# Kernel optimization log

Hardware: AMD Instinct MI355X
Metric: run time of the kernel (lower is better)

Reference implementation:

```python
import jax, jax.numpy as jnp
import numpy as np

N = 262144          # total views (rows of x)
G = 65536           # number of objects / view-groups (len(n_views))
D_IN, D_MID, D_GAT, D_OUT = 512, 256, 128, 256
BN_EPS = 1e-5
L2_EPS = 1e-9


def setup_inputs() -> dict:
    key = jax.random.key(0)
    ks = jax.random.split(key, 12)
    # post-backbone pooled features (dla34 last stage -> AdaptiveMaxPool2d(1) -> flatten)
    x = jax.random.normal(ks[0], (N, D_IN), jnp.float32)
    # ragged grouping: sorted segment ids, every segment guaranteed non-empty
    extra = jax.random.randint(ks[1], (N - G,), 0, G)
    seg_ids = jnp.sort(jnp.concatenate([jnp.arange(G), extra]).astype(jnp.int32))
    # sv_enc2: Linear(512,256) + BatchNorm1d (eval stats) + ReLU
    w2 = jax.random.normal(ks[2], (D_IN, D_MID), jnp.float32) * (D_IN ** -0.5)
    b2 = jnp.zeros((D_MID,), jnp.float32)
    bn_g = jnp.ones((D_MID,), jnp.float32)
    bn_b = jnp.zeros((D_MID,), jnp.float32)
    bn_m = jnp.zeros((D_MID,), jnp.float32)
    bn_v = jnp.ones((D_MID,), jnp.float32)
    # sv_enc3: Linear(256,128) + ReLU
    w3 = jax.random.normal(ks[3], (D_MID, D_GAT), jnp.float32) * (D_MID ** -0.5)
    b3 = jnp.zeros((D_GAT,), jnp.float32)
    # SelfGraphAttentionLinear(128, residual=True, dynamic_batching=True):
    # per-group attention pooling with residual
    gw = jax.random.normal(ks[4], (D_GAT, D_GAT), jnp.float32) * (D_GAT ** -0.5)
    gb = jnp.zeros((D_GAT,), jnp.float32)
    ga = jax.random.normal(ks[5], (D_GAT,), jnp.float32) * (D_GAT ** -0.5)
    # projection_head: Linear(128, 256), no activation
    pw = jax.random.normal(ks[6], (D_GAT, D_OUT), jnp.float32) * (D_GAT ** -0.5)
    pb = jnp.zeros((D_OUT,), jnp.float32)
    return {"x": x, "seg_ids": seg_ids, "w2": w2, "b2": b2,
            "bn_g": bn_g, "bn_b": bn_b, "bn_m": bn_m, "bn_v": bn_v,
            "w3": w3, "b3": b3, "gw": gw, "gb": gb, "ga": ga,
            "pw": pw, "pb": pb}


def reference(x, seg_ids, w2, b2, bn_g, bn_b, bn_m, bn_v, w3, b3, gw, gb, ga, pw, pb):
    # sv_enc2: Linear -> BN(eval) -> ReLU
    h = x @ w2 + b2
    h = bn_g * (h - bn_m) * jax.lax.rsqrt(bn_v + BN_EPS) + bn_b
    h = jax.nn.relu(h)
    # sv_enc3: Linear -> ReLU  -> [N, 128]
    h = jax.nn.relu(h @ w3 + b3)
    # GAT with dynamic batching: per-segment softmax attention pooling + residual
    g = h @ gw + gb                                    # [N, 128]
    e = g @ ga                                         # [N] attention logits
    m = jax.ops.segment_max(e, seg_ids, num_segments=G)
    w = jnp.exp(e - m[seg_ids])
    den = jax.ops.segment_sum(w, seg_ids, num_segments=G)
    alpha = w / den[seg_ids]                           # segment softmax
    pooled = jax.ops.segment_sum(alpha[:, None] * g, seg_ids, num_segments=G)
    h = jax.nn.relu(h + pooled[seg_ids])               # residual + gat_act
    # ragged per-group max pooling (the python loop in the original)
    obj = jax.ops.segment_max(h, seg_ids, num_segments=G)  # [G, 128]
    # projection head + L2 normalization
    out = obj @ pw + pb
    out = out / (jnp.linalg.norm(out, axis=1, keepdims=True) + L2_EPS)
    return out
```

## Files before the change

kernel.cpp:

```cpp
#include <hip/hip_runtime.h>
#include <hip/hip_bf16.h>
#include <stdint.h>

typedef __bf16 bf16;
typedef __bf16 bf16x2 __attribute__((ext_vector_type(2)));
typedef __bf16 bf16x4 __attribute__((ext_vector_type(4)));
typedef __bf16 bf16x8 __attribute__((ext_vector_type(8)));
typedef float  f32x4  __attribute__((ext_vector_type(4)));
typedef float  f32x2  __attribute__((ext_vector_type(2)));

#define NROWS 262144
#define GSEG  65536
#define DIN   512
#define DMID  256
#define DGAT  128
#define DOUT  256

#define OFF_W2S   0u
#define OFF_W3T   262144u
#define OFF_GWT   327680u
#define OFF_PWT   360448u
#define OFF_BNS   425984u
#define OFF_BNB   427008u
#define OFF_RS    428032u
#define OFF_H2    1048576u
#define OFF_G     68157440u
#define OFF_E     135266304u

#define GLOAD16(gptr, lptr) __builtin_amdgcn_global_load_lds( \
    (const __attribute__((address_space(1))) void*)(gptr),    \
    (__attribute__((address_space(3))) void*)(lptr), 16, 0, 0)

__global__ __launch_bounds__(256) void k_prep(
    const float* __restrict__ w2, const float* __restrict__ w3, const float* __restrict__ gw,
    const float* __restrict__ pw,
    const float* __restrict__ b2, const float* __restrict__ bn_g, const float* __restrict__ bn_b,
    const float* __restrict__ bn_m, const float* __restrict__ bn_v,
    bf16* __restrict__ w2s, bf16* __restrict__ w3t, bf16* __restrict__ gwt,
    bf16* __restrict__ pwt, float* __restrict__ bnS, float* __restrict__ bnB) {
  int idx = blockIdx.x * 256 + threadIdx.x;
  if (idx < DIN * DMID) {
    int k = idx / DMID, c = idx % DMID;
    int kk = k & 63, kb = k & ~63;
    w2s[c * DIN + kb + (kk ^ ((c & 7) << 3))] = (bf16)w2[idx];
  }
  if (idx < DMID * DGAT) {
    int k = idx / DGAT, c = idx % DGAT;
    w3t[c * DMID + k] = (bf16)w3[idx];
  }
  if (idx < DGAT * DGAT) {
    int k = idx / DGAT, c = idx % DGAT;
    gwt[c * DGAT + k] = (bf16)gw[idx];
  }
  if (idx < DOUT * DGAT) {
    int c = idx >> 7, k = idx & 127;
    pwt[idx] = (bf16)pw[k * DOUT + c];
  }
  if (idx < DMID) {
    float s = bn_g[idx] * rsqrtf(bn_v[idx] + 1e-5f);
    bnS[idx] = s;
    bnB[idx] = s * (b2[idx] - bn_m[idx]) + bn_b[idx];
  }
}

__global__ __launch_bounds__(256) void k_rowstart(const int* __restrict__ seg, int* __restrict__ rs) {
  int i = blockIdx.x * 256 + threadIdx.x;
  if (i >= NROWS) return;
  int s = seg[i];
  if (i == 0) rs[s] = 0;
  else if (seg[i - 1] != s) rs[s] = i;
  if (i == NROWS - 1) rs[GSEG] = NROWS;
}

__global__ __launch_bounds__(256, 3) void k_enc(
    const float* __restrict__ x, const bf16* __restrict__ w2s,
    const bf16* __restrict__ w3t, const bf16* __restrict__ gwt,
    const float* __restrict__ bnS, const float* __restrict__ bnB,
    const float* __restrict__ b3, const float* __restrict__ gb, const float* __restrict__ ga,
    bf16* __restrict__ h2, bf16* __restrict__ g, float* __restrict__ e) {
  __shared__ bf16 u[24576];
  __shared__ float eP[128];
  bf16* As  = u;
  bf16* Bs  = u + 4096;
  bf16* H1s = u;
  bf16* Hs  = u + 16384;
  bf16* Gs  = u;
  const int t = threadIdx.x;
  const int mBase = blockIdx.x * 64;
  const int w = t >> 6, l = t & 63;
  const int wm = w >> 1, wn = w & 1;
  const int l15 = l & 15, lh = l >> 4;
  const f32x4 zero = {0.f, 0.f, 0.f, 0.f};

  const int ar = t >> 2;
  const int ak = (t & 3) * 16;
  const float* xp = x + (size_t)(mBase + ar) * DIN + ak;
  const int aswz = (ar & 7) << 3;
  const int bcol0 = w * 64 + (l >> 3);
  const int bkk = (l & 7) * 8;

  f32x4 acc[4][4];
#pragma unroll
  for (int m = 0; m < 4; m++)
#pragma unroll
    for (int n = 0; n < 4; n++) acc[m][n] = zero;

  float4 pf[4];
#pragma unroll
  for (int j = 0; j < 4; j++) pf[j] = *(const float4*)(xp + j * 4);

  for (int kt = 0; kt < 8; ++kt) {
    bf16x8 av[2];
#pragma unroll
    for (int j = 0; j < 2; j++) {
      av[j][0] = (bf16)pf[2 * j].x; av[j][1] = (bf16)pf[2 * j].y;
      av[j][2] = (bf16)pf[2 * j].z; av[j][3] = (bf16)pf[2 * j].w;
      av[j][4] = (bf16)pf[2 * j + 1].x; av[j][5] = (bf16)pf[2 * j + 1].y;
      av[j][6] = (bf16)pf[2 * j + 1].z; av[j][7] = (bf16)pf[2 * j + 1].w;
    }
    __syncthreads();
    *(bf16x8*)(As + ar * 64 + ((ak + 0) ^ aswz)) = av[0];
    *(bf16x8*)(As + ar * 64 + ((ak + 8) ^ aswz)) = av[1];
#pragma unroll
    for (int i = 0; i < 8; i++) {
      GLOAD16(w2s + (size_t)(bcol0 + i * 8) * DIN + kt * 64 + bkk,
              Bs + (w * 8 + i) * 512);
    }
    __syncthreads();
    if (kt < 7) {
#pragma unroll
      for (int j = 0; j < 4; j++) pf[j] = *(const float4*)(xp + (kt + 1) * 64 + j * 4);
    }
#pragma unroll
    for (int ks = 0; ks < 2; ++ks) {
      const int kofs = ks * 32 + lh * 8;
      bf16x8 a[4], b[4];
#pragma unroll
      for (int m = 0; m < 4; m++) {
        int r = m * 16 + l15;
        a[m] = *(const bf16x8*)(As + r * 64 + (kofs ^ ((r & 7) << 3)));
      }
#pragma unroll
      for (int n = 0; n < 4; n++) {
        int c = w * 64 + n * 16 + l15;
        b[n] = *(const bf16x8*)(Bs + c * 64 + (kofs ^ ((c & 7) << 3)));
      }
#pragma unroll
      for (int m = 0; m < 4; m++)
#pragma unroll
        for (int n = 0; n < 4; n++)
          acc[m][n] = __builtin_amdgcn_mfma_f32_16x16x32_bf16(b[n], a[m], acc[m][n], 0, 0, 0);
    }
  }
  __syncthreads();

  const int rsw = (l15 & 7) << 3;
#pragma unroll
  for (int n = 0; n < 4; n++) {
    int c0 = w * 64 + n * 16 + lh * 4;
    f32x4 s4 = *(const f32x4*)(bnS + c0);
    f32x4 b4 = *(const f32x4*)(bnB + c0);
    int cs = (c0 & ~63) + ((c0 & 63) ^ rsw);
#pragma unroll
    for (int m = 0; m < 4; m++) {
      int rl = m * 16 + l15;
      bf16x4 o;
#pragma unroll
      for (int q = 0; q < 4; q++) {
        float v = acc[m][n][q] * s4[q] + b4[q];
        o[q] = (bf16)(v > 0.f ? v : 0.f);
      }
      *(bf16x4*)(H1s + rl * 256 + cs) = o;
    }
  }
  __syncthreads();

  f32x4 acc2[2][4];
#pragma unroll
  for (int m = 0; m < 2; m++)
#pragma unroll
    for (int n = 0; n < 4; n++) acc2[m][n] = zero;
#pragma unroll
  for (int ks = 0; ks < 8; ++ks) {
    const int kofs = ks * 32 + lh * 8;
    const int kb = kofs & ~63, kk = kofs & 63;
    bf16x8 a[2], b[4];
#pragma unroll
    for (int n = 0; n < 4; n++) {
      int c = wn * 64 + n * 16 + l15;
      b[n] = *(const bf16x8*)(w3t + (size_t)c * DMID + kofs);
    }
#pragma unroll
    for (int m = 0; m < 2; m++) {
      int r = wm * 32 + m * 16 + l15;
      a[m] = *(const bf16x8*)(H1s + r * 256 + kb + (kk ^ ((r & 7) << 3)));
    }
#pragma unroll
    for (int m = 0; m < 2; m++)
#pragma unroll
      for (int n = 0; n < 4; n++)
        acc2[m][n] = __builtin_amdgcn_mfma_f32_16x16x32_bf16(b[n], a[m], acc2[m][n], 0, 0, 0);
  }
#pragma unroll
  for (int n = 0; n < 4; n++) {
    int c0 = wn * 64 + n * 16 + lh * 4;
    f32x4 b4 = *(const f32x4*)(b3 + c0);
#pragma unroll
    for (int m = 0; m < 2; m++) {
      int rl = wm * 32 + m * 16 + l15;
      bf16x4 hb;
#pragma unroll
      for (int q = 0; q < 4; q++) {
        float v = acc2[m][n][q] + b4[q];
        hb[q] = (bf16)(v > 0.f ? v : 0.f);
      }
      *(bf16x4*)(Hs + rl * 128 + (c0 ^ ((rl & 7) << 3))) = hb;
    }
  }
  __syncthreads();

  f32x4 gacc[2][4];
#pragma unroll
  for (int m = 0; m < 2; m++)
#pragma unroll
    for (int n = 0; n < 4; n++) gacc[m][n] = zero;
#pragma unroll
  for (int ks = 0; ks < 4; ++ks) {
    const int kofs = ks * 32 + lh * 8;
    bf16x8 a[2], b[4];
#pragma unroll
    for (int n = 0; n < 4; n++) {
      int c = wn * 64 + n * 16 + l15;
      b[n] = *(const bf16x8*)(gwt + (size_t)c * DGAT + kofs);
    }
#pragma unroll
    for (int m = 0; m < 2; m++) {
      int r = wm * 32 + m * 16 + l15;
      a[m] = *(const bf16x8*)(Hs + r * 128 + (kofs ^ ((r & 7) << 3)));
    }
#pragma unroll
    for (int m = 0; m < 2; m++)
#pragma unroll
      for (int n = 0; n < 4; n++)
        gacc[m][n] = __builtin_amdgcn_mfma_f32_16x16x32_bf16(b[n], a[m], gacc[m][n], 0, 0, 0);
  }
  float ep[2] = {0.f, 0.f};
#pragma unroll
  for (int n = 0; n < 4; n++) {
    int c0 = wn * 64 + n * 16 + lh * 4;
    f32x4 gb4 = *(const f32x4*)(gb + c0);
    f32x4 ga4 = *(const f32x4*)(ga + c0);
#pragma unroll
    for (int m = 0; m < 2; m++) {
      int rl = wm * 32 + m * 16 + l15;
      bf16x4 gv;
#pragma unroll
      for (int q = 0; q < 4; q++) gv[q] = (bf16)(gacc[m][n][q] + gb4[q]);
      *(bf16x4*)(Gs + rl * 128 + (c0 ^ ((rl & 7) << 3))) = gv;
#pragma unroll
      for (int q = 0; q < 4; q++) ep[m] += (float)gv[q] * ga4[q];
    }
  }
#pragma unroll
  for (int m = 0; m < 2; m++) {
    float v = ep[m];
    v += __shfl_xor(v, 16, 64);
    v += __shfl_xor(v, 32, 64);
    if (l < 16) eP[(wm * 32 + m * 16 + l) * 2 + wn] = v;
  }
  __syncthreads();

  const int drow = t >> 4;
  const int dc = (t & 15) * 8;
#pragma unroll
  for (int i = 0; i < 4; ++i) {
    int rl = i * 16 + drow;
    int cs = dc ^ ((rl & 7) << 3);
    *(bf16x8*)(h2 + (size_t)(mBase + rl) * DGAT + dc) = *(const bf16x8*)(Hs + rl * 128 + cs);
    *(bf16x8*)(g  + (size_t)(mBase + rl) * DGAT + dc) = *(const bf16x8*)(Gs + rl * 128 + cs);
  }
  if (t < 64) e[mBase + t] = eP[t * 2] + eP[t * 2 + 1];
}

__global__ __launch_bounds__(256) void k_segproj(
    const float* __restrict__ e, const bf16* __restrict__ g, const bf16* __restrict__ h2,
    const int* __restrict__ rs, const bf16* __restrict__ pwt, const float* __restrict__ pb,
    float* __restrict__ out) {
  __shared__ bf16 objs[16 * 128];
  __shared__ float red[16 * 4];
  const int t = threadIdx.x;
  const int w = t >> 6, l = t & 63;
  const int l15 = l & 15, lh = l >> 4;
  const int gBase = blockIdx.x * 16;
  const f32x4 zero = {0.f, 0.f, 0.f, 0.f};

#pragma unroll
  for (int j = 0; j < 4; ++j) {
    const int sl = w * 4 + j;
    const int s = gBase + sl;
    const int r0 = rs[s], r1 = rs[s + 1];
    float m = -3.4e38f, den = 0.f;
    f32x2 p = {0.f, 0.f};
    for (int r = r0; r < r1; ++r) {
      float ev = e[r];
      float mn = fmaxf(m, ev);
      float cor = __expf(m - mn);
      float wr = __expf(ev - mn);
      den = den * cor + wr;
      bf16x2 gv = *(const bf16x2*)(g + (size_t)r * DGAT + l * 2);
      p[0] = p[0] * cor + wr * (float)gv[0];
      p[1] = p[1] * cor + wr * (float)gv[1];
      m = mn;
    }
    float inv = 1.f / den;
    p[0] *= inv; p[1] *= inv;
    f32x2 om = {0.f, 0.f};
    for (int r = r0; r < r1; ++r) {
      bf16x2 hv = *(const bf16x2*)(h2 + (size_t)r * DGAT + l * 2);
      om[0] = fmaxf(om[0], fmaxf((float)hv[0] + p[0], 0.f));
      om[1] = fmaxf(om[1], fmaxf((float)hv[1] + p[1], 0.f));
    }
    bf16x2 ob;
    ob[0] = (bf16)om[0];
    ob[1] = (bf16)om[1];
    int k2 = (l * 2) ^ ((sl & 7) << 3);
    *(bf16x2*)(objs + sl * 128 + k2) = ob;
  }
  __syncthreads();

  f32x4 acc[4];
#pragma unroll
  for (int n = 0; n < 4; n++) acc[n] = zero;
#pragma unroll
  for (int ks = 0; ks < 4; ++ks) {
    const int kofs = ks * 32 + lh * 8;
    bf16x8 a = *(const bf16x8*)(objs + l15 * 128 + (kofs ^ ((l15 & 7) << 3)));
#pragma unroll
    for (int n = 0; n < 4; n++) {
      int c = w * 64 + n * 16 + l15;
      bf16x8 b = *(const bf16x8*)(pwt + (size_t)c * DGAT + kofs);
      acc[n] = __builtin_amdgcn_mfma_f32_16x16x32_bf16(b, a, acc[n], 0, 0, 0);
    }
  }
  float s2 = 0.f;
#pragma unroll
  for (int n = 0; n < 4; n++) {
    int c0 = w * 64 + n * 16 + lh * 4;
    f32x4 p4 = *(const f32x4*)(pb + c0);
#pragma unroll
    for (int q = 0; q < 4; q++) {
      acc[n][q] += p4[q];
      s2 += acc[n][q] * acc[n][q];
    }
  }
  s2 += __shfl_xor(s2, 16, 64);
  s2 += __shfl_xor(s2, 32, 64);
  if (l < 16) red[l * 4 + w] = s2;
  __syncthreads();
  float tot = red[l15 * 4 + 0] + red[l15 * 4 + 1] + red[l15 * 4 + 2] + red[l15 * 4 + 3];
  float rinv = 1.f / (sqrtf(tot) + 1e-9f);
#pragma unroll
  for (int n = 0; n < 4; n++) {
    int c0 = w * 64 + n * 16 + lh * 4;
    f32x4 o;
#pragma unroll
    for (int q = 0; q < 4; q++) o[q] = acc[n][q] * rinv;
    *(f32x4*)(out + (size_t)(gBase + l15) * DOUT + c0) = o;
  }
}

extern "C" void kernel_launch(void* const* d_in, const int* in_sizes, int n_in,
                              void* d_out, int out_size, void* d_ws, size_t ws_size,
                              hipStream_t stream) {
  const float* x    = (const float*)d_in[0];
  const int*   seg  = (const int*)d_in[1];
  const float* w2   = (const float*)d_in[2];
  const float* b2   = (const float*)d_in[3];
  const float* bn_g = (const float*)d_in[4];
  const float* bn_b = (const float*)d_in[5];
  const float* bn_m = (const float*)d_in[6];
  const float* bn_v = (const float*)d_in[7];
  const float* w3   = (const float*)d_in[8];
  const float* b3   = (const float*)d_in[9];
  const float* gw   = (const float*)d_in[10];
  const float* gb   = (const float*)d_in[11];
  const float* ga   = (const float*)d_in[12];
  const float* pw   = (const float*)d_in[13];
  const float* pb   = (const float*)d_in[14];

  char* ws = (char*)d_ws;
  bf16*  w2s = (bf16*)(ws + OFF_W2S);
  bf16*  w3t = (bf16*)(ws + OFF_W3T);
  bf16*  gwt = (bf16*)(ws + OFF_GWT);
  bf16*  pwt = (bf16*)(ws + OFF_PWT);
  float* bnS = (float*)(ws + OFF_BNS);
  float* bnB = (float*)(ws + OFF_BNB);
  int*   rs  = (int*)(ws + OFF_RS);
  bf16*  h2  = (bf16*)(ws + OFF_H2);
  bf16*  g   = (bf16*)(ws + OFF_G);
  float* e   = (float*)(ws + OFF_E);
  float* out = (float*)d_out;

  k_prep<<<512, 256, 0, stream>>>(w2, w3, gw, pw, b2, bn_g, bn_b, bn_m, bn_v,
                                  w2s, w3t, gwt, pwt, bnS, bnB);
  k_rowstart<<<NROWS / 256, 256, 0, stream>>>(seg, rs);
  k_enc<<<NROWS / 64, 256, 0, stream>>>(x, w2s, w3t, gwt, bnS, bnB, b3, gb, ga, h2, g, e);
  k_segproj<<<GSEG / 16, 256, 0, stream>>>(e, g, h2, rs, pwt, pb, out);
}
```

Before: 343.7 us.

## Double-buffer W2 tiles in encoder GEMM and interleave segment loops

The encoder kernel gets a second LDS buffer for the W2 tiles. The next k-tile's weights are prefetched right after the barrier, so the global load overlaps the current MFMA step. This raises LDS use and drops launch bounds from 3 to 2 blocks per CU, which lowers occupancy. Separately, the segment kernel now walks its four segments per wave in lockstep instead of one after another, so more independent loads are in flight.

Result: slower. 371.5 us (+8.1%).

```diff
diff --git a/kernel.cpp b/kernel.cpp
--- a/kernel.cpp
+++ b/kernel.cpp
@@ -72,18 +72,20 @@
   if (i == NROWS - 1) rs[GSEG] = NROWS;
 }
 
-__global__ __launch_bounds__(256, 3) void k_enc(
+__global__ __launch_bounds__(256, 2) void k_enc(
     const float* __restrict__ x, const bf16* __restrict__ w2s,
     const bf16* __restrict__ w3t, const bf16* __restrict__ gwt,
     const float* __restrict__ bnS, const float* __restrict__ bnB,
     const float* __restrict__ b3, const float* __restrict__ gb, const float* __restrict__ ga,
     bf16* __restrict__ h2, bf16* __restrict__ g, float* __restrict__ e) {
-  __shared__ bf16 u[24576];
+  __shared__ bf16 u[36864];
   __shared__ float eP[128];
-  bf16* As  = u;
-  bf16* Bs  = u + 4096;
+  bf16* As   = u;
+  bf16* BsArr[2];
+  BsArr[0] = u + 4096;
+  BsArr[1] = u + 20480;
   bf16* H1s = u;
-  bf16* Hs  = u + 16384;
+  bf16* Hs  = u + 20480;
   bf16* Gs  = u;
   const int t = threadIdx.x;
   const int mBase = blockIdx.x * 64;
@@ -108,8 +110,15 @@
   float4 pf[4];
 #pragma unroll
   for (int j = 0; j < 4; j++) pf[j] = *(const float4*)(xp + j * 4);
+#pragma unroll
+  for (int i = 0; i < 8; i++) {
+    GLOAD16(w2s + (size_t)(bcol0 + i * 8) * DIN + 0 * 64 + bkk,
+            BsArr[0] + (w * 8 + i) * 512);
+  }
 
   for (int kt = 0; kt < 8; ++kt) {
+    const int cur = kt & 1;
+    const bf16* Bs = BsArr[cur];
     bf16x8 av[2];
 #pragma unroll
     for (int j = 0; j < 2; j++) {
@@ -121,15 +130,15 @@
     __syncthreads();
     *(bf16x8*)(As + ar * 64 + ((ak + 0) ^ aswz)) = av[0];
     *(bf16x8*)(As + ar * 64 + ((ak + 8) ^ aswz)) = av[1];
-#pragma unroll
-    for (int i = 0; i < 8; i++) {
-      GLOAD16(w2s + (size_t)(bcol0 + i * 8) * DIN + kt * 64 + bkk,
-              Bs + (w * 8 + i) * 512);
-    }
     __syncthreads();
     if (kt < 7) {
 #pragma unroll
       for (int j = 0; j < 4; j++) pf[j] = *(const float4*)(xp + (kt + 1) * 64 + j * 4);
+#pragma unroll
+      for (int i = 0; i < 8; i++) {
+        GLOAD16(w2s + (size_t)(bcol0 + i * 8) * DIN + (kt + 1) * 64 + bkk,
+                BsArr[cur ^ 1] + (w * 8 + i) * 512);
+      }
     }
 #pragma unroll
     for (int ks = 0; ks < 2; ++ks) {
@@ -294,37 +303,64 @@
   const int gBase = blockIdx.x * 16;
   const f32x4 zero = {0.f, 0.f, 0.f, 0.f};
 
-#pragma unroll
-  for (int j = 0; j < 4; ++j) {
-    const int sl = w * 4 + j;
-    const int s = gBase + sl;
-    const int r0 = rs[s], r1 = rs[s + 1];
-    float m = -3.4e38f, den = 0.f;
-    f32x2 p = {0.f, 0.f};
-    for (int r = r0; r < r1; ++r) {
-      float ev = e[r];
-      float mn = fmaxf(m, ev);
-      float cor = __expf(m - mn);
-      float wr = __expf(ev - mn);
-      den = den * cor + wr;
-      bf16x2 gv = *(const bf16x2*)(g + (size_t)r * DGAT + l * 2);
-      p[0] = p[0] * cor + wr * (float)gv[0];
-      p[1] = p[1] * cor + wr * (float)gv[1];
-      m = mn;
-    }
-    float inv = 1.f / den;
-    p[0] *= inv; p[1] *= inv;
-    f32x2 om = {0.f, 0.f};
-    for (int r = r0; r < r1; ++r) {
-      bf16x2 hv = *(const bf16x2*)(h2 + (size_t)r * DGAT + l * 2);
-      om[0] = fmaxf(om[0], fmaxf((float)hv[0] + p[0], 0.f));
-      om[1] = fmaxf(om[1], fmaxf((float)hv[1] + p[1], 0.f));
-    }
-    bf16x2 ob;
-    ob[0] = (bf16)om[0];
-    ob[1] = (bf16)om[1];
-    int k2 = (l * 2) ^ ((sl & 7) << 3);
-    *(bf16x2*)(objs + sl * 128 + k2) = ob;
+  {
+    const int s0 = gBase + w * 4;
+    int r0[4], len[4];
+    int maxlen = 0;
+#pragma unroll
+    for (int j = 0; j < 4; ++j) {
+      r0[j] = rs[s0 + j];
+      len[j] = rs[s0 + j + 1] - r0[j];
+      maxlen = max(maxlen, len[j]);
+    }
+    float mx[4] = {-3.4e38f, -3.4e38f, -3.4e38f, -3.4e38f};
+    float den[4] = {0.f, 0.f, 0.f, 0.f};
+    f32x2 p[4];
+#pragma unroll
+    for (int j = 0; j < 4; ++j) { p[j][0] = 0.f; p[j][1] = 0.f; }
+    for (int i = 0; i < maxlen; ++i) {
+#pragma unroll
+      for (int j = 0; j < 4; ++j)
+        if (i < len[j]) {
+          int r = r0[j] + i;
+          float ev = e[r];
+          float mn = fmaxf(mx[j], ev);
+          float cor = __expf(mx[j] - mn);
+          float wr = __expf(ev - mn);
+          den[j] = den[j] * cor + wr;
+          bf16x2 gv = *(const bf16x2*)(g + (size_t)r * DGAT + l * 2);
+          p[j][0] = p[j][0] * cor + wr * (float)gv[0];
+          p[j][1] = p[j][1] * cor + wr * (float)gv[1];
+          mx[j] = mn;
+        }
+    }
+#pragma unroll
+    for (int j = 0; j < 4; ++j) {
+      float inv = 1.f / den[j];
+      p[j][0] *= inv; p[j][1] *= inv;
+    }
+    f32x2 om[4];
+#pragma unroll
+    for (int j = 0; j < 4; ++j) { om[j][0] = 0.f; om[j][1] = 0.f; }
+    for (int i = 0; i < maxlen; ++i) {
+#pragma unroll
+      for (int j = 0; j < 4; ++j)
+        if (i < len[j]) {
+          int r = r0[j] + i;
+          bf16x2 hv = *(const bf16x2*)(h2 + (size_t)r * DGAT + l * 2);
+          om[j][0] = fmaxf(om[j][0], fmaxf((float)hv[0] + p[j][0], 0.f));
+          om[j][1] = fmaxf(om[j][1], fmaxf((float)hv[1] + p[j][1], 0.f));
+        }
+    }
+#pragma unroll
+    for (int j = 0; j < 4; ++j) {
+      const int sl = w * 4 + j;
+      bf16x2 ob;
+      ob[0] = (bf16)om[j][0];
+      ob[1] = (bf16)om[j][1];
+      int k2 = (l * 2) ^ ((sl & 7) << 3);
+      *(bf16x2*)(objs + sl * 128 + k2) = ob;
+    }
   }
   __syncthreads();
 
```
